# Optimization experiments

Measured on AMD Instinct MI355X. Metric: run time of the kernel, lower is better.

The kernel has to match this reference:

```python
import jax, jax.numpy as jnp
import numpy as np

B, C, H, W = 32, 1536, 24, 24
HID, D, K = 512, 128, 64  # hidden, cluster_dim, num_clusters


def setup_inputs() -> dict:
    key = jax.random.key(0)
    ks = jax.random.split(key, 6)
    def rn(k, shape, scale):
        return jax.random.normal(k, shape, dtype=jnp.float32) * scale
    return {
        "x": rn(ks[0], (B, C, H, W), 1.0),
        # cluster_features: Conv2d(C,512,1) -> ReLU -> Conv2d(512,D,1)
        "w1c": rn(ks[1], (HID, C), 0.02), "b1c": jnp.zeros((HID,), jnp.float32),
        "w2c": rn(ks[2], (D, HID), 0.02), "b2c": jnp.zeros((D,), jnp.float32),
        # score: Conv2d(C,512,1) -> ReLU -> Conv2d(512,K,1)
        "w1s": rn(ks[3], (HID, C), 0.02), "b1s": jnp.zeros((HID,), jnp.float32),
        "w2s": rn(ks[4], (K, HID), 0.02), "b2s": jnp.zeros((K,), jnp.float32),
        "temperature": jnp.array(1.0, jnp.float32),
    }


def _sinkhorn_log(S, num_iters=3):
    # log-domain OT solver with uniform marginals log(1/n), reg=1 (M/reg == M)
    b, m, n = S.shape
    norm = -jnp.log(jnp.asarray(n, S.dtype))
    log_a = jnp.full((b, m), norm, S.dtype)
    log_b = jnp.full((b, n), norm, S.dtype)
    u = jnp.zeros((b, m), S.dtype)
    v = jnp.zeros((b, n), S.dtype)
    for _ in range(num_iters):
        u = log_a - jax.nn.logsumexp(S + v[:, None, :], axis=2)
        v = log_b - jax.nn.logsumexp(S + u[:, :, None], axis=1)
    # get_matching_probs subtracts norm at the end
    return S + u[:, :, None] + v[:, None, :] - norm


def reference(x, w1c, b1c, w2c, b2c, w1s, b1s, w2s, b2s, temperature):
    b, c, h, w = x.shape
    xf = x.reshape(b, c, h * w)  # (B, C, N); 1x1 conv == channel GEMM
    # cluster features f: (B, D, N)
    hc = jax.nn.relu(jnp.einsum('oc,bcn->bon', w1c, xf) + b1c[None, :, None])
    f = jnp.einsum('oc,bcn->bon', w2c, hc) + b2c[None, :, None]
    # assignment scores p: (B, K, N)
    hs = jax.nn.relu(jnp.einsum('oc,bcn->bon', w1s, xf) + b1s[None, :, None])
    s = jnp.einsum('oc,bcn->bon', w2s, hs) + b2s[None, :, None]
    log_p = _sinkhorn_log(s, num_iters=3)
    p = jnp.exp(log_p / temperature) + jnp.exp(log_p)  # (B, K, N)
    # (f.unsqueeze(2) * p.unsqueeze(1)).sum(-1) == batched matmul
    agg = jnp.einsum('bcn,bkn->bck', f, p)  # (B, D, K)
    flat = agg.reshape(b, -1)
    nrm = jnp.maximum(jnp.linalg.norm(flat, axis=-1, keepdims=True), 1e-12)
    return flat / nrm
```

## Files before the change

### kernel.cpp

```cpp
#include <hip/hip_runtime.h>

typedef unsigned short ushort_t;
typedef float f32x4 __attribute__((ext_vector_type(4)));
typedef short short8 __attribute__((ext_vector_type(8)));

#define B_   32
#define C_   1536
#define N_   576
#define HID_ 512
#define D_   128
#define K_   64

__device__ __forceinline__ float bf2f(ushort_t u) {
    union { unsigned u; float f; } c; c.u = ((unsigned)u) << 16; return c.f;
}
__device__ __forceinline__ ushort_t f2bf(float x) {
    unsigned u = __float_as_uint(x);
    return (ushort_t)((u + 0x7FFFu + ((u >> 16) & 1u)) >> 16);
}

typedef const __attribute__((address_space(1))) char gas_char;
typedef __attribute__((address_space(3))) char las_char;
__device__ __forceinline__ void cp16(const void* g, void* l) {
    __builtin_amdgcn_global_load_lds((gas_char*)(size_t)g,
                                     (las_char*)(unsigned)(size_t)l, 16, 0, 0);
}

#define OB1_  1572864
#define OW2C_ 1573888
#define OB2C_ 1639424
#define OW2S_ 1639552
#define OB2S_ 1672320
#define WTOT_ 1672384
#define TRB_  6912
#define CVB_  ((WTOT_ + 255) / 256)

__global__ __launch_bounds__(256) void prep_kernel(
    const void* __restrict__ x,
    const void* __restrict__ w1c, const void* __restrict__ b1c,
    const void* __restrict__ w2c, const void* __restrict__ b2c,
    const void* __restrict__ w1s, const void* __restrict__ b1s,
    const void* __restrict__ w2s, const void* __restrict__ b2s,
    const unsigned* __restrict__ temp,
    ushort_t* __restrict__ xt, ushort_t* __restrict__ o, float* __restrict__ Tp)
{
    __shared__ ushort_t t[64][68];
    unsigned d = temp[0];
    int flag = (d == 0x3F800000u) ? 1 : 0;
    int tid = threadIdx.x;
    int idx = blockIdx.x;
    if (idx == 0 && tid == 0)
        *Tp = flag ? __uint_as_float(d) : bf2f((ushort_t)(d & 0xFFFFu));

    if (idx < TRB_) {
        int b = idx / 216, rem = idx % 216;
        int c0 = (rem % 24) * 64, n0 = (rem / 24) * 64;
        ushort_t* xtb = xt + (size_t)b * N_ * C_;
        int r = tid >> 4, c4 = (tid & 15) * 4;
        if (flag) {
            const float* xb = (const float*)x + (size_t)b * C_ * N_;
#pragma unroll
            for (int i = 0; i < 4; ++i) {
                int cc = r + i * 16;
                float4 v = *(const float4*)&xb[(size_t)(c0 + cc) * N_ + n0 + c4];
                t[cc][c4 + 0] = f2bf(v.x);
                t[cc][c4 + 1] = f2bf(v.y);
                t[cc][c4 + 2] = f2bf(v.z);
                t[cc][c4 + 3] = f2bf(v.w);
            }
        } else {
            const ushort_t* xb = (const ushort_t*)x + (size_t)b * C_ * N_;
#pragma unroll
            for (int i = 0; i < 4; ++i) {
                int cc = r + i * 16;
                *(uint2*)&t[cc][c4] =
                    *(const uint2*)&xb[(size_t)(c0 + cc) * N_ + n0 + c4];
            }
        }
        __syncthreads();
#pragma unroll
        for (int i = 0; i < 4; ++i) {
            int nn = r + i * 16;
            ushort_t v0 = t[c4 + 0][nn], v1 = t[c4 + 1][nn];
            ushort_t v2 = t[c4 + 2][nn], v3 = t[c4 + 3][nn];
            uint2 vv;
            vv.x = (unsigned)v0 | ((unsigned)v1 << 16);
            vv.y = (unsigned)v2 | ((unsigned)v3 << 16);
            *(uint2*)&xtb[(size_t)(n0 + nn) * C_ + c0 + c4] = vv;
        }
    } else {
        int i = (idx - TRB_) * 256 + tid;
        if (i >= WTOT_) return;
        const void* p; int off;
        if      (i < 786432)  { p = w1c; off = i; }
        else if (i < OB1_)    { p = w1s; off = i - 786432; }
        else if (i < 1573376) { p = b1c; off = i - OB1_; }
        else if (i < OW2C_)   { p = b1s; off = i - 1573376; }
        else if (i < OB2C_)   { p = w2c; off = i - OW2C_; }
        else if (i < OW2S_)   { p = b2c; off = i - OB2C_; }
        else if (i < OB2S_)   { p = w2s; off = i - OW2S_; }
        else                  { p = b2s; off = i - OB2S_; }
        o[i] = flag ? f2bf(((const float*)p)[off]) : ((const ushort_t*)p)[off];
    }
}

__global__ __launch_bounds__(256) void gemm1_kernel(
    const ushort_t* __restrict__ Xt, const ushort_t* __restrict__ W1,
    const ushort_t* __restrict__ bias, ushort_t* __restrict__ h)
{
    __shared__ ushort_t Atile[128 * 32];
    __shared__ ushort_t Btile[128 * 32];
    int idx = blockIdx.x;
    int g = (idx & 7) + ((idx >> 6) << 3);
    int t = (idx >> 3) & 7;
    int mt = g % 5, b = g / 5;
    int row0 = mt * 128, col0 = t * 128;

    int tid = threadIdx.x, w = tid >> 6, lane = tid & 63;
    int wr = w >> 1, wc = w & 1;
    int r16 = lane & 15, q = lane >> 4, kh = q * 8;

    const ushort_t* A = Xt + (size_t)b * N_ * C_;
    int ar0 = min(row0 + (tid >> 2), N_ - 1);
    int ar1 = min(row0 + 64 + (tid >> 2), N_ - 1);
    const ushort_t* ag0 = A + (size_t)ar0 * C_ + (tid & 3) * 8;
    const ushort_t* ag1 = A + (size_t)ar1 * C_ + (tid & 3) * 8;
    const ushort_t* bg0 = W1 + (size_t)(col0 + (tid >> 2)) * C_ + (tid & 3) * 8;
    const ushort_t* bg1 = bg0 + (size_t)64 * C_;
    ushort_t* lA0 = &Atile[w * 512];
    ushort_t* lA1 = &Atile[2048 + w * 512];
    ushort_t* lB0 = &Btile[w * 512];
    ushort_t* lB1 = &Btile[2048 + w * 512];

    f32x4 acc[4][4];
#pragma unroll
    for (int i = 0; i < 4; ++i)
#pragma unroll
        for (int j = 0; j < 4; ++j) acc[i][j] = f32x4{0.f, 0.f, 0.f, 0.f};

    for (int k0 = 0; k0 < C_; k0 += 32) {
        cp16(ag0, lA0); cp16(ag1, lA1);
        cp16(bg0, lB0); cp16(bg1, lB1);
        ag0 += 32; ag1 += 32; bg0 += 32; bg1 += 32;
        __syncthreads();
        short8 af[4], bf[4];
#pragma unroll
        for (int i = 0; i < 4; ++i)
            af[i] = *(const short8*)&Atile[(wr * 64 + i * 16 + r16) * 32 + kh];
#pragma unroll
        for (int j = 0; j < 4; ++j)
            bf[j] = *(const short8*)&Btile[(wc * 64 + j * 16 + r16) * 32 + kh];
#pragma unroll
        for (int i = 0; i < 4; ++i)
#pragma unroll
            for (int j = 0; j < 4; ++j)
                acc[i][j] = __builtin_amdgcn_mfma_f32_16x16x32_bf16(
                    af[i], bf[j], acc[i][j], 0, 0, 0);
        __syncthreads();
    }
    ushort_t* hb = h + (size_t)b * N_ * 1024;
#pragma unroll
    for (int j = 0; j < 4; ++j) {
        int col = col0 + wc * 64 + j * 16 + r16;
        float cb = bf2f(bias[col]);
#pragma unroll
        for (int i = 0; i < 4; ++i) {
            int rowb = row0 + wr * 64 + i * 16 + q * 4;
#pragma unroll
            for (int r = 0; r < 4; ++r) {
                int rr = rowb + r;
                if (rr < N_) {
                    float v = fmaxf(acc[i][j][r] + cb, 0.f);
                    hb[(size_t)rr * 1024 + col] = f2bf(v);
                }
            }
        }
    }
}

__global__ __launch_bounds__(256) void gemm2_kernel(
    const ushort_t* __restrict__ Wb, const ushort_t* __restrict__ h,
    ushort_t* __restrict__ fbuf, float* __restrict__ sbuf)
{
    __shared__ ushort_t Atile[128 * 32];
    __shared__ ushort_t Btile[128 * 32];
    int nt = blockIdx.x, b = blockIdx.y, z = blockIdx.z;
    int col0 = nt * 128;
    int Mclamp = z ? K_ : D_;
    const ushort_t* Aw   = Wb + (z ? OW2S_ : OW2C_);
    const ushort_t* bias = Wb + (z ? OB2S_ : OB2C_);
    const ushort_t* hb = h + (size_t)b * N_ * 1024 + (z ? 512 : 0);

    int tid = threadIdx.x, w = tid >> 6, lane = tid & 63;
    int wr = w >> 1, wc = w & 1;
    int r16 = lane & 15, q = lane >> 4, kh = q * 8;

    int ar0 = min((tid >> 2), Mclamp - 1);
    int ar1 = min(64 + (tid >> 2), Mclamp - 1);
    const ushort_t* ag0 = Aw + (size_t)ar0 * HID_ + (tid & 3) * 8;
    const ushort_t* ag1 = Aw + (size_t)ar1 * HID_ + (tid & 3) * 8;
    int br0 = min(col0 + (tid >> 2), N_ - 1);
    int br1 = min(col0 + 64 + (tid >> 2), N_ - 1);
    const ushort_t* bg0 = hb + (size_t)br0 * 1024 + (tid & 3) * 8;
    const ushort_t* bg1 = hb + (size_t)br1 * 1024 + (tid & 3) * 8;
    ushort_t* lA0 = &Atile[w * 512];
    ushort_t* lA1 = &Atile[2048 + w * 512];
    ushort_t* lB0 = &Btile[w * 512];
    ushort_t* lB1 = &Btile[2048 + w * 512];

    f32x4 acc[4][4];
#pragma unroll
    for (int i = 0; i < 4; ++i)
#pragma unroll
        for (int j = 0; j < 4; ++j) acc[i][j] = f32x4{0.f, 0.f, 0.f, 0.f};

    for (int k0 = 0; k0 < HID_; k0 += 32) {
        cp16(ag0, lA0); cp16(ag1, lA1);
        cp16(bg0, lB0); cp16(bg1, lB1);
        ag0 += 32; ag1 += 32; bg0 += 32; bg1 += 32;
        __syncthreads();
        short8 af[4], bf[4];
#pragma unroll
        for (int i = 0; i < 4; ++i)
            af[i] = *(const short8*)&Atile[(wr * 64 + i * 16 + r16) * 32 + kh];
#pragma unroll
        for (int j = 0; j < 4; ++j)
            bf[j] = *(const short8*)&Btile[(wc * 64 + j * 16 + r16) * 32 + kh];
#pragma unroll
        for (int i = 0; i < 4; ++i)
#pragma unroll
            for (int j = 0; j < 4; ++j)
                acc[i][j] = __builtin_amdgcn_mfma_f32_16x16x32_bf16(
                    af[i], bf[j], acc[i][j], 0, 0, 0);
        __syncthreads();
    }
#pragma unroll
    for (int j = 0; j < 4; ++j) {
        int col = col0 + wc * 64 + j * 16 + r16;
#pragma unroll
        for (int i = 0; i < 4; ++i) {
            int rowb = wr * 64 + i * 16 + q * 4;
#pragma unroll
            for (int r = 0; r < 4; ++r) {
                int rr = rowb + r;
                if (rr < Mclamp && col < N_) {
                    float v = acc[i][j][r] + bf2f(bias[rr]);
                    if (z == 0)
                        fbuf[(size_t)b * D_ * N_ + (size_t)rr * N_ + col] = f2bf(v);
                    else
                        sbuf[(size_t)b * K_ * N_ + (size_t)rr * N_ + col] = v;
                }
            }
        }
    }
}

__global__ __launch_bounds__(256) void tail_kernel(
    const ushort_t* __restrict__ f_all, const float* __restrict__ s_all,
    const float* __restrict__ Tp, const unsigned* __restrict__ temp,
    void* __restrict__ out)
{
    int b = blockIdx.x;
    const float* S = s_all + (size_t)b * K_ * N_;
    __shared__ float su[K_];
    __shared__ float sv[N_];
    __shared__ ushort_t Ftile[128 * 32];
    __shared__ ushort_t Ptile[64 * 32];
    __shared__ float red[4];
    int tid = threadIdx.x, w = tid >> 6, lane = tid & 63;
    int r16 = lane & 15, q = lane >> 4, kh = q * 8;
    const float norm = -logf((float)N_);

    for (int n = tid; n < N_; n += 256) sv[n] = 0.f;
    __syncthreads();

    for (int it = 0; it < 3; ++it) {
        for (int r = w; r < K_; r += 4) {
            const float* Sr = S + r * N_;
            float a0 = 0.f, a1 = 0.f, a2 = 0.f;
#pragma unroll
            for (int k = 0; k < 9; k += 3) {
                int n0 = lane + 64 * k;
                a0 += __expf(Sr[n0] + sv[n0]);
                a1 += __expf(Sr[n0 + 64] + sv[n0 + 64]);
                a2 += __expf(Sr[n0 + 128] + sv[n0 + 128]);
            }
            float t = a0 + a1 + a2;
#pragma unroll
            for (int off = 32; off; off >>= 1) t += __shfl_xor(t, off);
            if (lane == 0) su[r] = norm - __logf(t);
        }
        __syncthreads();
        for (int n = tid; n < N_; n += 256) {
            const float* Sc = S + n;
            float a0 = 0.f, a1 = 0.f, a2 = 0.f, a3 = 0.f;
#pragma unroll
            for (int m = 0; m < K_; m += 4) {
                a0 += __expf(Sc[(m + 0) * N_] + su[m + 0]);
                a1 += __expf(Sc[(m + 1) * N_] + su[m + 1]);
                a2 += __expf(Sc[(m + 2) * N_] + su[m + 2]);
                a3 += __expf(Sc[(m + 3) * N_] + su[m + 3]);
            }
            sv[n] = norm - __logf((a0 + a1) + (a2 + a3));
        }
        __syncthreads();
    }

    float invT = 1.f / (*Tp);
    const ushort_t* f = f_all + (size_t)b * D_ * N_;
    int prow = tid >> 2, pc0 = (tid & 3) * 8;
    float urow = su[prow];
    const ushort_t* fg0 = f + (size_t)(tid >> 2) * N_ + (tid & 3) * 8;
    const ushort_t* fg1 = f + (size_t)(64 + (tid >> 2)) * N_ + (tid & 3) * 8;
    ushort_t* lF0 = &Ftile[w * 512];
    ushort_t* lF1 = &Ftile[2048 + w * 512];
    const float* Srow = S + (size_t)prow * N_ + pc0;

    f32x4 acc[2][4];
#pragma unroll
    for (int i = 0; i < 2; ++i)
#pragma unroll
        for (int j = 0; j < 4; ++j) acc[i][j] = f32x4{0.f, 0.f, 0.f, 0.f};

    for (int s = 0; s < 18; ++s) {
        cp16(fg0, lF0); cp16(fg1, lF1);
        fg0 += 32; fg1 += 32;
        int nb = s * 32;
        ushort_t pv[8];
#pragma unroll
        for (int e = 0; e < 8; ++e) {
            float lp = Srow[e] + urow + sv[nb + pc0 + e] - norm;
            pv[e] = f2bf(__expf(lp * invT) + __expf(lp));
        }
        Srow += 32;
        uint2 w0, w1;
        w0.x = (unsigned)pv[0] | ((unsigned)pv[1] << 16);
        w0.y = (unsigned)pv[2] | ((unsigned)pv[3] << 16);
        w1.x = (unsigned)pv[4] | ((unsigned)pv[5] << 16);
        w1.y = (unsigned)pv[6] | ((unsigned)pv[7] << 16);
        *(uint2*)&Ptile[prow * 32 + pc0] = w0;
        *(uint2*)&Ptile[prow * 32 + pc0 + 4] = w1;
        __syncthreads();
        short8 af[2], bf[4];
#pragma unroll
        for (int i = 0; i < 2; ++i)
            af[i] = *(const short8*)&Ftile[(w * 32 + i * 16 + r16) * 32 + kh];
#pragma unroll
        for (int j = 0; j < 4; ++j)
            bf[j] = *(const short8*)&Ptile[(j * 16 + r16) * 32 + kh];
#pragma unroll
        for (int i = 0; i < 2; ++i)
#pragma unroll
            for (int j = 0; j < 4; ++j)
                acc[i][j] = __builtin_amdgcn_mfma_f32_16x16x32_bf16(
                    af[i], bf[j], acc[i][j], 0, 0, 0);
        __syncthreads();
    }

    float ssq = 0.f;
#pragma unroll
    for (int i = 0; i < 2; ++i)
#pragma unroll
        for (int j = 0; j < 4; ++j)
#pragma unroll
            for (int r = 0; r < 4; ++r) { float v = acc[i][j][r]; ssq += v * v; }
#pragma unroll
    for (int off = 32; off; off >>= 1) ssq += __shfl_xor(ssq, off);
    if (lane == 0) red[w] = ssq;
    __syncthreads();
    float tot = red[0] + red[1] + red[2] + red[3];
    float inv = 1.f / fmaxf(sqrtf(tot), 1e-12f);
    int flag = (temp[0] == 0x3F800000u) ? 1 : 0;
#pragma unroll
    for (int i = 0; i < 2; ++i) {
#pragma unroll
        for (int j = 0; j < 4; ++j) {
            int col = j * 16 + r16;
#pragma unroll
            for (int r = 0; r < 4; ++r) {
                int row = w * 32 + i * 16 + q * 4 + r;
                float v = acc[i][j][r] * inv;
                size_t idx = (size_t)b * D_ * K_ + (size_t)row * K_ + col;
                if (flag) ((float*)out)[idx] = v;
                else      ((ushort_t*)out)[idx] = f2bf(v);
            }
        }
    }
}

extern "C" void kernel_launch(void* const* d_in, const int* in_sizes, int n_in,
                              void* d_out, int out_size, void* d_ws, size_t ws_size,
                              hipStream_t stream) {
    const void* x    = d_in[0];
    const void* w1c  = d_in[1];
    const void* b1c  = d_in[2];
    const void* w2c  = d_in[3];
    const void* b2c  = d_in[4];
    const void* w1s  = d_in[5];
    const void* b1s  = d_in[6];
    const void* w2s  = d_in[7];
    const void* b2s  = d_in[8];
    const unsigned* temp = (const unsigned*)d_in[9];

    char* ws = (char*)d_ws;
    float* Tp = (float*)ws;
    ushort_t* Wb = (ushort_t*)(ws + 256);
    size_t offXt = 256 + (((size_t)WTOT_ * 2 + 255) & ~(size_t)255);
    ushort_t* Xt = (ushort_t*)(ws + offXt);
    size_t xtBytes = (size_t)B_ * N_ * C_ * 2;
    ushort_t* h  = (ushort_t*)(ws + offXt + xtBytes);
    size_t o0 = offXt;
    ushort_t* fbuf = (ushort_t*)(ws + o0);  o0 += (size_t)B_ * D_ * N_ * 2;
    float*    sbuf = (float*)(ws + o0);     o0 += (size_t)B_ * K_ * N_ * 4;

    prep_kernel<<<dim3(TRB_ + CVB_), 256, 0, stream>>>(
        x, w1c, b1c, w2c, b2c, w1s, b1s, w2s, b2s, temp, Xt, Wb, Tp);
    gemm1_kernel<<<dim3(1280), 256, 0, stream>>>(Xt, Wb, Wb + OB1_, h);
    gemm2_kernel<<<dim3(5, B_, 2), 256, 0, stream>>>(Wb, h, fbuf, sbuf);
    tail_kernel<<<dim3(B_), 256, 0, stream>>>(fbuf, sbuf, Tp, temp, (void*)d_out);
}
```

Measured before the change: 349.4 us.

## Flatten gemm1 over batch rows, widen K-step with swizzled LDS, double tail threads

gemm1 now treats the batch and spatial dimensions as one flat M dimension (18432 rows = 144 tiles of 128), which removes the padded partial tiles and drops the grid from 1280 to 1152 blocks. Each K-step now covers 64 instead of 32, halving the number of barriers, and uses an XOR-swizzled LDS layout to avoid bank conflicts. The block index is remapped so that consecutive blocks share weight tiles. The tail kernel moves to 512 threads, giving the Sinkhorn reductions and the final aggregation GEMM twice the parallelism per batch. In exchange gemm1 uses twice the LDS per block, which may lower occupancy.

```diff
diff --git a/kernel.cpp b/kernel.cpp
--- a/kernel.cpp
+++ b/kernel.cpp
@@ -108,29 +108,28 @@
     const ushort_t* __restrict__ Xt, const ushort_t* __restrict__ W1,
     const ushort_t* __restrict__ bias, ushort_t* __restrict__ h)
 {
-    __shared__ ushort_t Atile[128 * 32];
-    __shared__ ushort_t Btile[128 * 32];
+    __shared__ ushort_t Atile[128 * 64];
+    __shared__ ushort_t Btile[128 * 64];
     int idx = blockIdx.x;
-    int g = (idx & 7) + ((idx >> 6) << 3);
-    int t = (idx >> 3) & 7;
-    int mt = g % 5, b = g / 5;
+    int l = (idx & 7) * 144 + (idx >> 3);
+    int mt = l >> 3, t = l & 7;
     int row0 = mt * 128, col0 = t * 128;
 
     int tid = threadIdx.x, w = tid >> 6, lane = tid & 63;
     int wr = w >> 1, wc = w & 1;
     int r16 = lane & 15, q = lane >> 4, kh = q * 8;
 
-    const ushort_t* A = Xt + (size_t)b * N_ * C_;
-    int ar0 = min(row0 + (tid >> 2), N_ - 1);
-    int ar1 = min(row0 + 64 + (tid >> 2), N_ - 1);
-    const ushort_t* ag0 = A + (size_t)ar0 * C_ + (tid & 3) * 8;
-    const ushort_t* ag1 = A + (size_t)ar1 * C_ + (tid & 3) * 8;
-    const ushort_t* bg0 = W1 + (size_t)(col0 + (tid >> 2)) * C_ + (tid & 3) * 8;
-    const ushort_t* bg1 = bg0 + (size_t)64 * C_;
-    ushort_t* lA0 = &Atile[w * 512];
-    ushort_t* lA1 = &Atile[2048 + w * 512];
-    ushort_t* lB0 = &Btile[w * 512];
-    ushort_t* lB1 = &Btile[2048 + w * 512];
+    int srow = tid >> 3;
+    int cx = ((tid & 7) ^ (srow & 7)) * 8;
+    const ushort_t* ag[4];
+    const ushort_t* bg[4];
+#pragma unroll
+    for (int s = 0; s < 4; ++s) {
+        ag[s] = Xt + (size_t)(row0 + s * 32 + srow) * C_ + cx;
+        bg[s] = W1 + (size_t)(col0 + s * 32 + srow) * C_ + cx;
+    }
+    ushort_t* lA = &Atile[tid * 8];
+    ushort_t* lB = &Btile[tid * 8];
 
     f32x4 acc[4][4];
 #pragma unroll
@@ -138,41 +137,48 @@
 #pragma unroll
         for (int j = 0; j < 4; ++j) acc[i][j] = f32x4{0.f, 0.f, 0.f, 0.f};
 
-    for (int k0 = 0; k0 < C_; k0 += 32) {
-        cp16(ag0, lA0); cp16(ag1, lA1);
-        cp16(bg0, lB0); cp16(bg1, lB1);
-        ag0 += 32; ag1 += 32; bg0 += 32; bg1 += 32;
-        __syncthreads();
-        short8 af[4], bf[4];
-#pragma unroll
-        for (int i = 0; i < 4; ++i)
-            af[i] = *(const short8*)&Atile[(wr * 64 + i * 16 + r16) * 32 + kh];
-#pragma unroll
-        for (int j = 0; j < 4; ++j)
-            bf[j] = *(const short8*)&Btile[(wc * 64 + j * 16 + r16) * 32 + kh];
-#pragma unroll
-        for (int i = 0; i < 4; ++i)
+    int rowa = wr * 64 + r16;
+    int rowb = wc * 64 + r16;
+    int xr = (r16 & 7) * 8;
+
+    for (int k0 = 0; k0 < C_; k0 += 64) {
+#pragma unroll
+        for (int s = 0; s < 4; ++s) {
+            cp16(ag[s], lA + s * 2048);
+            cp16(bg[s], lB + s * 2048);
+            ag[s] += 64; bg[s] += 64;
+        }
+        __syncthreads();
+#pragma unroll
+        for (int ks = 0; ks < 2; ++ks) {
+            int ke = (ks * 32 + kh) ^ xr;
+            short8 af[4], bf[4];
+#pragma unroll
+            for (int i = 0; i < 4; ++i)
+                af[i] = *(const short8*)&Atile[(rowa + i * 16) * 64 + ke];
 #pragma unroll
             for (int j = 0; j < 4; ++j)
-                acc[i][j] = __builtin_amdgcn_mfma_f32_16x16x32_bf16(
-                    af[i], bf[j], acc[i][j], 0, 0, 0);
-        __syncthreads();
-    }
-    ushort_t* hb = h + (size_t)b * N_ * 1024;
+                bf[j] = *(const short8*)&Btile[(rowb + j * 16) * 64 + ke];
+#pragma unroll
+            for (int i = 0; i < 4; ++i)
+#pragma unroll
+                for (int j = 0; j < 4; ++j)
+                    acc[i][j] = __builtin_amdgcn_mfma_f32_16x16x32_bf16(
+                        af[i], bf[j], acc[i][j], 0, 0, 0);
+        }
+        __syncthreads();
+    }
 #pragma unroll
     for (int j = 0; j < 4; ++j) {
         int col = col0 + wc * 64 + j * 16 + r16;
         float cb = bf2f(bias[col]);
 #pragma unroll
         for (int i = 0; i < 4; ++i) {
-            int rowb = row0 + wr * 64 + i * 16 + q * 4;
+            int rowo = row0 + wr * 64 + i * 16 + q * 4;
 #pragma unroll
             for (int r = 0; r < 4; ++r) {
-                int rr = rowb + r;
-                if (rr < N_) {
-                    float v = fmaxf(acc[i][j][r] + cb, 0.f);
-                    hb[(size_t)rr * 1024 + col] = f2bf(v);
-                }
+                float v = fmaxf(acc[i][j][r] + cb, 0.f);
+                h[(size_t)(rowo + r) * 1024 + col] = f2bf(v);
             }
         }
     }
@@ -255,7 +261,7 @@
     }
 }
 
-__global__ __launch_bounds__(256) void tail_kernel(
+__global__ __launch_bounds__(512) void tail_kernel(
     const ushort_t* __restrict__ f_all, const float* __restrict__ s_all,
     const float* __restrict__ Tp, const unsigned* __restrict__ temp,
     void* __restrict__ out)
@@ -266,16 +272,16 @@
     __shared__ float sv[N_];
     __shared__ ushort_t Ftile[128 * 32];
     __shared__ ushort_t Ptile[64 * 32];
-    __shared__ float red[4];
+    __shared__ float red[8];
     int tid = threadIdx.x, w = tid >> 6, lane = tid & 63;
     int r16 = lane & 15, q = lane >> 4, kh = q * 8;
     const float norm = -logf((float)N_);
 
-    for (int n = tid; n < N_; n += 256) sv[n] = 0.f;
+    for (int n = tid; n < N_; n += 512) sv[n] = 0.f;
     __syncthreads();
 
     for (int it = 0; it < 3; ++it) {
-        for (int r = w; r < K_; r += 4) {
+        for (int r = w; r < K_; r += 8) {
             const float* Sr = S + r * N_;
             float a0 = 0.f, a1 = 0.f, a2 = 0.f;
 #pragma unroll
@@ -291,7 +297,7 @@
             if (lane == 0) su[r] = norm - __logf(t);
         }
         __syncthreads();
-        for (int n = tid; n < N_; n += 256) {
+        for (int n = tid; n < N_; n += 512) {
             const float* Sc = S + n;
             float a0 = 0.f, a1 = 0.f, a2 = 0.f, a3 = 0.f;
 #pragma unroll
@@ -308,82 +314,67 @@
 
     float invT = 1.f / (*Tp);
     const ushort_t* f = f_all + (size_t)b * D_ * N_;
-    int prow = tid >> 2, pc0 = (tid & 3) * 8;
+    const ushort_t* fg = f + (size_t)(tid >> 2) * N_ + (tid & 3) * 8;
+    ushort_t* lF = &Ftile[tid * 8];
+    int prow = tid >> 3, pc0 = (tid & 7) * 4;
     float urow = su[prow];
-    const ushort_t* fg0 = f + (size_t)(tid >> 2) * N_ + (tid & 3) * 8;
-    const ushort_t* fg1 = f + (size_t)(64 + (tid >> 2)) * N_ + (tid & 3) * 8;
-    ushort_t* lF0 = &Ftile[w * 512];
-    ushort_t* lF1 = &Ftile[2048 + w * 512];
     const float* Srow = S + (size_t)prow * N_ + pc0;
 
-    f32x4 acc[2][4];
-#pragma unroll
-    for (int i = 0; i < 2; ++i)
-#pragma unroll
-        for (int j = 0; j < 4; ++j) acc[i][j] = f32x4{0.f, 0.f, 0.f, 0.f};
+    f32x4 acc[4];
+#pragma unroll
+    for (int j = 0; j < 4; ++j) acc[j] = f32x4{0.f, 0.f, 0.f, 0.f};
 
     for (int s = 0; s < 18; ++s) {
-        cp16(fg0, lF0); cp16(fg1, lF1);
-        fg0 += 32; fg1 += 32;
+        cp16(fg, lF);
+        fg += 32;
         int nb = s * 32;
-        ushort_t pv[8];
-#pragma unroll
-        for (int e = 0; e < 8; ++e) {
+        ushort_t pv[4];
+#pragma unroll
+        for (int e = 0; e < 4; ++e) {
             float lp = Srow[e] + urow + sv[nb + pc0 + e] - norm;
             pv[e] = f2bf(__expf(lp * invT) + __expf(lp));
         }
         Srow += 32;
-        uint2 w0, w1;
+        uint2 w0;
         w0.x = (unsigned)pv[0] | ((unsigned)pv[1] << 16);
         w0.y = (unsigned)pv[2] | ((unsigned)pv[3] << 16);
-        w1.x = (unsigned)pv[4] | ((unsigned)pv[5] << 16);
-        w1.y = (unsigned)pv[6] | ((unsigned)pv[7] << 16);
         *(uint2*)&Ptile[prow * 32 + pc0] = w0;
-        *(uint2*)&Ptile[prow * 32 + pc0 + 4] = w1;
-        __syncthreads();
-        short8 af[2], bf[4];
-#pragma unroll
-        for (int i = 0; i < 2; ++i)
-            af[i] = *(const short8*)&Ftile[(w * 32 + i * 16 + r16) * 32 + kh];
+        __syncthreads();
+        short8 af = *(const short8*)&Ftile[(w * 16 + r16) * 32 + kh];
+        short8 bf[4];
 #pragma unroll
         for (int j = 0; j < 4; ++j)
             bf[j] = *(const short8*)&Ptile[(j * 16 + r16) * 32 + kh];
 #pragma unroll
-        for (int i = 0; i < 2; ++i)
-#pragma unroll
-            for (int j = 0; j < 4; ++j)
-                acc[i][j] = __builtin_amdgcn_mfma_f32_16x16x32_bf16(
-                    af[i], bf[j], acc[i][j], 0, 0, 0);
+        for (int j = 0; j < 4; ++j)
+            acc[j] = __builtin_amdgcn_mfma_f32_16x16x32_bf16(
+                af, bf[j], acc[j], 0, 0, 0);
         __syncthreads();
     }
 
     float ssq = 0.f;
 #pragma unroll
-    for (int i = 0; i < 2; ++i)
-#pragma unroll
-        for (int j = 0; j < 4; ++j)
-#pragma unroll
-            for (int r = 0; r < 4; ++r) { float v = acc[i][j][r]; ssq += v * v; }
+    for (int j = 0; j < 4; ++j)
+#pragma unroll
+        for (int r = 0; r < 4; ++r) { float v = acc[j][r]; ssq += v * v; }
 #pragma unroll
     for (int off = 32; off; off >>= 1) ssq += __shfl_xor(ssq, off);
     if (lane == 0) red[w] = ssq;
     __syncthreads();
-    float tot = red[0] + red[1] + red[2] + red[3];
+    float tot = (red[0] + red[1] + red[2] + red[3])
+              + (red[4] + red[5] + red[6] + red[7]);
     float inv = 1.f / fmaxf(sqrtf(tot), 1e-12f);
     int flag = (temp[0] == 0x3F800000u) ? 1 : 0;
 #pragma unroll
-    for (int i = 0; i < 2; ++i) {
-#pragma unroll
-        for (int j = 0; j < 4; ++j) {
-            int col = j * 16 + r16;
-#pragma unroll
-            for (int r = 0; r < 4; ++r) {
-                int row = w * 32 + i * 16 + q * 4 + r;
-                float v = acc[i][j][r] * inv;
-                size_t idx = (size_t)b * D_ * K_ + (size_t)row * K_ + col;
-                if (flag) ((float*)out)[idx] = v;
-                else      ((ushort_t*)out)[idx] = f2bf(v);
-            }
+    for (int j = 0; j < 4; ++j) {
+        int col = j * 16 + r16;
+#pragma unroll
+        for (int r = 0; r < 4; ++r) {
+            int row = w * 16 + q * 4 + r;
+            float v = acc[j][r] * inv;
+            size_t idx = (size_t)b * D_ * K_ + (size_t)row * K_ + col;
+            if (flag) ((float*)out)[idx] = v;
+            else      ((ushort_t*)out)[idx] = f2bf(v);
         }
     }
 }
@@ -415,7 +406,7 @@
 
     prep_kernel<<<dim3(TRB_ + CVB_), 256, 0, stream>>>(
         x, w1c, b1c, w2c, b2c, w1s, b1s, w2s, b2s, temp, Xt, Wb, Tp);
-    gemm1_kernel<<<dim3(1280), 256, 0, stream>>>(Xt, Wb, Wb + OB1_, h);
+    gemm1_kernel<<<dim3(1152), 256, 0, stream>>>(Xt, Wb, Wb + OB1_, h);
     gemm2_kernel<<<dim3(5, B_, 2), 256, 0, stream>>>(Wb, h, fbuf, sbuf);
-    tail_kernel<<<dim3(B_), 256, 0, stream>>>(fbuf, sbuf, Tp, temp, (void*)d_out);
-}
+    tail_kernel<<<dim3(B_), 512, 0, stream>>>(fbuf, sbuf, Tp, temp, (void*)d_out);
+}
```

New measurement: 326.7 us. -6.5%, faster.
